# Kernel optimization log

Hardware: AMD Instinct MI355X
Metric: run time of the kernel (lower is better)

Reference implementation:

```python
import jax, jax.numpy as jnp
import numpy as np

HIDDEN = 1024
NUM_HEADS = 16
HEAD_DIM = HIDDEN // NUM_HEADS
ROPE_THETA = 10000.0


def rope_tables(seq_len, head_dim, theta):
    inv_freq = 1.0 / theta ** (jnp.arange(0, head_dim, 2, dtype=jnp.float32) / head_dim)
    pos = jnp.arange(seq_len, dtype=jnp.float32)
    freqs = jnp.outer(pos, inv_freq)  # [S, hd/2]
    return jnp.cos(freqs), jnp.sin(freqs)


def apply_rope(x, cos, sin):
    # x: [B, nh, S, hd]; cos/sin: [S, hd/2]
    x1, x2 = jnp.split(x, 2, axis=-1)
    return jnp.concatenate([x1 * cos - x2 * sin, x2 * cos + x1 * sin], axis=-1)


def setup_inputs() -> dict:
    key = jax.random.key(0)
    k1, k2, k3 = jax.random.split(key, 3)
    B, S = 2, 2048
    hidden_states = jax.random.normal(k1, (B, S, HIDDEN), dtype=jnp.float32)
    # nn.Linear stores weight as [out, in]; y = x @ W.T
    Wqkv = jax.random.normal(k2, (3 * HIDDEN, HIDDEN), dtype=jnp.float32) * (HIDDEN ** -0.5)
    Wo = jax.random.normal(k3, (HIDDEN, HIDDEN), dtype=jnp.float32) * (HIDDEN ** -0.5)
    return {"hidden_states": hidden_states, "Wqkv": Wqkv, "Wo": Wo}


def reference(hidden_states, Wqkv, Wo):
    B, S, H = hidden_states.shape
    qkv = hidden_states @ Wqkv.T  # [B, S, 3H]
    qkv = qkv.reshape(B, S, 3, NUM_HEADS, HEAD_DIM)
    q, k, v = jnp.moveaxis(qkv, 2, 0)  # each [B, S, nh, hd]
    q = jnp.transpose(q, (0, 2, 1, 3))  # [B, nh, S, hd]
    k = jnp.transpose(k, (0, 2, 1, 3))
    v = jnp.transpose(v, (0, 2, 1, 3))
    cos, sin = rope_tables(S, HEAD_DIM, ROPE_THETA)
    q = apply_rope(q, cos, sin)
    k = apply_rope(k, cos, sin)
    scale = 1.0 / jnp.sqrt(jnp.asarray(HEAD_DIM, dtype=q.dtype))
    scores = jnp.einsum("bhqd,bhkd->bhqk", q, k) * scale
    causal = jnp.tril(jnp.ones((S, S), dtype=bool))
    scores = jnp.where(causal, scores, jnp.finfo(scores.dtype).min)
    attn = jax.nn.softmax(scores, axis=-1)
    out = jnp.einsum("bhqk,bhkd->bhqd", attn, v)  # [B, nh, S, hd]
    out = jnp.transpose(out, (0, 2, 1, 3)).reshape(B, S, H)
    return out @ Wo.T
```

## Files before the change

### kernel.cpp

```cpp
#include <hip/hip_runtime.h>
#include <hip/hip_bf16.h>
#include <math.h>

typedef __bf16 bf16_t;
typedef __attribute__((ext_vector_type(8))) __bf16 bf16x8;
typedef __attribute__((ext_vector_type(4))) float f32x4;
typedef __attribute__((ext_vector_type(16))) float f32x16;
typedef __attribute__((ext_vector_type(4))) unsigned u32x4;

#define AS1(p) ((__attribute__((address_space(1))) void*)(p))
#define AS3(p) ((__attribute__((address_space(3))) void*)(p))

__global__ void cvt_f32_bf16(const float* __restrict__ in, bf16_t* __restrict__ out, int n8) {
  int i = blockIdx.x * blockDim.x + threadIdx.x;
  if (i >= n8) return;
  const float4* p = (const float4*)in;
  float4 a = p[2 * i], b = p[2 * i + 1];
  bf16x8 o;
  o[0] = (bf16_t)a.x; o[1] = (bf16_t)a.y; o[2] = (bf16_t)a.z; o[3] = (bf16_t)a.w;
  o[4] = (bf16_t)b.x; o[5] = (bf16_t)b.y; o[6] = (bf16_t)b.z; o[7] = (bf16_t)b.w;
  ((bf16x8*)out)[i] = o;
}

__global__ void rope_tables_k(float* __restrict__ cosb, float* __restrict__ sinb) {
  int t = blockIdx.x * 256 + threadIdx.x;
  int s = t >> 5, i = t & 31;
  float inv = powf(10000.0f, -(float)i / 32.0f);
  float ang = (float)s * inv;
  float sv, cv;
  sincosf(ang, &sv, &cv);
  cosb[t] = cv;
  sinb[t] = sv;
}

__global__ __launch_bounds__(256)
void pack_rope(bf16_t* __restrict__ qkv, const float* __restrict__ cosb,
               const float* __restrict__ sinb, bf16_t* __restrict__ Kp) {
  __shared__ bf16_t vl[64][72];
  const int t = blockIdx.x, bh = blockIdx.y, b = bh >> 4, h = bh & 15;
  const int tid = threadIdx.x;
  const int r = tid >> 2, j = tid & 3;
  const int s = t * 64 + r;
  bf16_t* base = qkv + ((size_t)(b * 2048 + s)) * 3072 + h * 64;
  const float* cb = cosb + s * 32 + j * 8;
  const float* sb = sinb + s * 32 + j * 8;
  bf16x8 q1 = *(const bf16x8*)(base + j * 8);
  bf16x8 q2 = *(const bf16x8*)(base + j * 8 + 32);
  bf16x8 k1 = *(const bf16x8*)(base + 1024 + j * 8);
  bf16x8 k2 = *(const bf16x8*)(base + 1024 + j * 8 + 32);
  bf16x8 v1 = *(const bf16x8*)(base + 2048 + j * 8);
  bf16x8 v2 = *(const bf16x8*)(base + 2048 + j * 8 + 32);
  const float QS = 0.125f * 1.4426950408889634f;
  bf16x8 qo1, qo2, ko1, ko2;
#pragma unroll
  for (int i = 0; i < 8; ++i) {
    float c = cb[i], sn = sb[i];
    float a1 = (float)q1[i], a2 = (float)q2[i];
    qo1[i] = (bf16_t)((a1 * c - a2 * sn) * QS);
    qo2[i] = (bf16_t)((a2 * c + a1 * sn) * QS);
    float b1 = (float)k1[i], b2 = (float)k2[i];
    ko1[i] = (bf16_t)(b1 * c - b2 * sn);
    ko2[i] = (bf16_t)(b2 * c + b1 * sn);
  }
  *(bf16x8*)(base + j * 8) = qo1;
  *(bf16x8*)(base + j * 8 + 32) = qo2;
  bf16_t* kd = Kp + ((size_t)(bh * 32 + t)) * 4096 + r * 64;
  *(bf16x8*)(kd + ((j ^ (r & 7)) * 8)) = ko1;
  *(bf16x8*)(kd + (((j + 4) ^ (r & 7)) * 8)) = ko2;
#pragma unroll
  for (int i = 0; i < 8; ++i) { vl[r][j * 8 + i] = v1[i]; vl[r][j * 8 + 32 + i] = v2[i]; }
  __syncthreads();
  const int d = r;
  bf16x8 o1, o2;
#pragma unroll
  for (int i = 0; i < 8; ++i) { o1[i] = vl[j * 16 + i][d]; o2[i] = vl[j * 16 + 8 + i][d]; }
  bf16_t* vd = base + 2048;
  *(bf16x8*)(vd + (((2 * j) ^ (d & 7)) * 8)) = o1;
  *(bf16x8*)(vd + (((2 * j + 1) ^ (d & 7)) * 8)) = o2;
}

template <typename OutT>
__global__ __launch_bounds__(256, 2)
void gemm_nt(const bf16_t* __restrict__ A, const bf16_t* __restrict__ B,
             OutT* __restrict__ C, int M, int N, int K) {
  __shared__ __align__(16) bf16_t lA[128 * 64];
  __shared__ __align__(16) bf16_t lB[128 * 64];
  const int tid = threadIdx.x;
  const int wid = tid >> 6, lane = tid & 63;
  const int lr = lane & 15, lg = lane >> 4;
  const int nwg = gridDim.x * gridDim.y;
  int lin = blockIdx.y * gridDim.x + blockIdx.x;
  lin = (lin & 7) * (nwg >> 3) + (lin >> 3);
  const int m0 = (lin / gridDim.x) * 128, n0 = (lin % gridDim.x) * 128;
  const int wm = (wid >> 1) * 64, wn = (wid & 1) * 64;
  const int srow = lane >> 3;
  const int scol = (lane & 7) * 8;
  f32x4 acc[4][4];
#pragma unroll
  for (int i = 0; i < 4; ++i)
#pragma unroll
    for (int j = 0; j < 4; ++j) acc[i][j] = f32x4{0.f, 0.f, 0.f, 0.f};

  const int nk = K >> 6;
  for (int kt = 0; kt < nk; ++kt) {
    const int k0 = kt << 6;
    __syncthreads();
#pragma unroll
    for (int i = 0; i < 4; ++i) {
      int c = (wid << 2) + i;
      int r = (c << 3) + srow;
      __builtin_amdgcn_global_load_lds(AS1(A + (size_t)(m0 + r) * K + k0 + scol),
                                       AS3(&lA[c * 512]), 16, 0, 0);
      __builtin_amdgcn_global_load_lds(AS1(B + (size_t)(n0 + r) * K + k0 + scol),
                                       AS3(&lB[c * 512]), 16, 0, 0);
    }
    __syncthreads();
#pragma unroll
    for (int ks = 0; ks < 2; ++ks) {
      bf16x8 af[4], bfr[4];
#pragma unroll
      for (int i = 0; i < 4; ++i) {
        af[i]  = *(const bf16x8*)&lA[(wm + i * 16 + lr) * 64 + ks * 32 + lg * 8];
        bfr[i] = *(const bf16x8*)&lB[(wn + i * 16 + lr) * 64 + ks * 32 + lg * 8];
      }
#pragma unroll
      for (int i = 0; i < 4; ++i)
#pragma unroll
        for (int j = 0; j < 4; ++j)
          acc[i][j] = __builtin_amdgcn_mfma_f32_16x16x32_bf16(af[i], bfr[j], acc[i][j], 0, 0, 0);
    }
  }
#pragma unroll
  for (int i = 0; i < 4; ++i)
#pragma unroll
    for (int j = 0; j < 4; ++j)
#pragma unroll
      for (int r = 0; r < 4; ++r) {
        int row = m0 + wm + i * 16 + lg * 4 + r;
        int col = n0 + wn + j * 16 + lr;
        C[(size_t)row * N + col] = (OutT)acc[i][j][r];
      }
}

__device__ inline unsigned pkbf(float a, float b) {
  bf16_t x = (bf16_t)a, y = (bf16_t)b;
  return (unsigned)__builtin_bit_cast(unsigned short, x) |
         ((unsigned)__builtin_bit_cast(unsigned short, y) << 16);
}
__device__ inline f32x16 zero16() {
  f32x16 z;
#pragma unroll
  for (int r = 0; r < 16; ++r) z[r] = 0.f;
  return z;
}

__global__ __launch_bounds__(128, 1)
void attn_fwd(const bf16_t* __restrict__ qkv, const bf16_t* __restrict__ Kp,
              bf16_t* __restrict__ O) {
  __shared__ __align__(16) bf16_t Ksh[2][4096];
  __shared__ __align__(16) bf16_t Vsh[2][4096];
  const int tid = threadIdx.x, wid = tid >> 6, lane = tid & 63;
  const int ln = lane & 31, h = lane >> 5;
  const int lin = blockIdx.y * 16 + blockIdx.x;
  const int c = (lin >> 3) & 15;
  const int bh = (lin & 7) | ((lin >> 7) << 3);
  const int b = bh >> 4, hd = bh & 15;
  const int cA = c, cB = 31 - c;
  const int NI = 33;

  const bf16_t* QArow = qkv + ((size_t)(b * 2048 + cA * 64 + wid * 32 + ln)) * 3072 + hd * 64;
  const bf16_t* QBrow = qkv + ((size_t)(b * 2048 + cB * 64 + wid * 32 + ln)) * 3072 + hd * 64;
  bf16x8 qA[4], qB[4], qc[4];
#pragma unroll
  for (int t = 0; t < 4; ++t) {
    qA[t] = *(const bf16x8*)(QArow + t * 16 + h * 8);
    qB[t] = *(const bf16x8*)(QBrow + t * 16 + h * 8);
    qc[t] = qA[t];
  }
  int qwc = cA * 64 + wid * 32;

  f32x16 o0 = zero16(), o1 = zero16();
  float lp = 0.f;

  const bf16_t* Kbase = Kp + ((size_t)bh * 32) * 4096 + tid * 8;
  const bf16_t* Vbase = qkv + ((size_t)(b * 2048 + (tid >> 3))) * 3072 + 2048 + hd * 64 + (tid & 7) * 8;

#define TILE_OF(IT) ((IT) <= c ? (IT) : (IT) - (c + 1))
#define STAGE(IT, BUF)                                                                    \
  do {                                                                                    \
    int _t = TILE_OF(IT);                                                                 \
    const bf16_t* ks = Kbase + (size_t)_t * 4096;                                         \
    __builtin_amdgcn_global_load_lds(AS1(ks),        AS3(&Ksh[BUF][tid * 8]), 16, 0, 0);  \
    __builtin_amdgcn_global_load_lds(AS1(ks + 1024), AS3(&Ksh[BUF][1024 + tid * 8]), 16, 0, 0); \
    __builtin_amdgcn_global_load_lds(AS1(ks + 2048), AS3(&Ksh[BUF][2048 + tid * 8]), 16, 0, 0); \
    __builtin_amdgcn_global_load_lds(AS1(ks + 3072), AS3(&Ksh[BUF][3072 + tid * 8]), 16, 0, 0); \
    const bf16_t* vs = Vbase + (size_t)_t * 64 * 3072;                                    \
    __builtin_amdgcn_global_load_lds(AS1(vs),             AS3(&Vsh[BUF][tid * 8]), 16, 0, 0);        \
    __builtin_amdgcn_global_load_lds(AS1(vs + 16 * 3072), AS3(&Vsh[BUF][1024 + tid * 8]), 16, 0, 0); \
    __builtin_amdgcn_global_load_lds(AS1(vs + 32 * 3072), AS3(&Vsh[BUF][2048 + tid * 8]), 16, 0, 0); \
    __builtin_amdgcn_global_load_lds(AS1(vs + 48 * 3072), AS3(&Vsh[BUF][3072 + tid * 8]), 16, 0, 0); \
  } while (0)

  STAGE(0, 0);
  for (int i = 0; i < NI; ++i) {
    asm volatile("s_waitcnt vmcnt(0)" ::: "memory");
    __builtin_amdgcn_s_barrier();
    if (i + 1 < NI) STAGE(i + 1, (i + 1) & 1);
    const bf16_t* K = &Ksh[i & 1][0];
    const bf16_t* V = &Vsh[i & 1][0];
    f32x16 s0 = zero16(), s1 = zero16();
    __builtin_amdgcn_s_setprio(1);
#pragma unroll
    for (int t = 0; t < 4; ++t) {
      const int ch = 2 * t + h;
      bf16x8 k0 = *(const bf16x8*)&K[ln * 64 + ((ch ^ (ln & 7)) * 8)];
      bf16x8 k1 = *(const bf16x8*)&K[(32 + ln) * 64 + ((ch ^ (ln & 7)) * 8)];
      s0 = __builtin_amdgcn_mfma_f32_32x32x16_bf16(k0, qc[t], s0, 0, 0, 0);
      s1 = __builtin_amdgcn_mfma_f32_32x32x16_bf16(k1, qc[t], s1, 0, 0, 0);
    }
    __builtin_amdgcn_s_setprio(0);
    if (i == c || i == NI - 1) {
      int qg = qwc + ln;
      int k0g = TILE_OF(i) * 64;
#pragma unroll
      for (int r = 0; r < 16; ++r) {
        int kv = k0g + (r & 3) + 8 * (r >> 2) + 4 * h;
        if (kv > qg) s0[r] = -3e38f;
        if (kv + 32 > qg) s1[r] = -3e38f;
      }
    }
#pragma unroll
    for (int r = 0; r < 16; ++r) {
      float p0 = __builtin_amdgcn_exp2f(s0[r]); lp += p0; s0[r] = p0;
      float p1 = __builtin_amdgcn_exp2f(s1[r]); lp += p1; s1[r] = p1;
    }
    __builtin_amdgcn_s_setprio(1);
#pragma unroll
    for (int t = 0; t < 4; ++t) {
      const int u = t & 1;
      f32x16 sv = (t >> 1) ? s1 : s0;
      unsigned x  = pkbf(sv[8 * u + 0], sv[8 * u + 1]);
      unsigned x2 = pkbf(sv[8 * u + 2], sv[8 * u + 3]);
      unsigned y  = pkbf(sv[8 * u + 4], sv[8 * u + 5]);
      unsigned y2 = pkbf(sv[8 * u + 6], sv[8 * u + 7]);
      asm volatile("v_permlane32_swap_b32 %0, %1" : "+v"(x), "+v"(y));
      asm volatile("v_permlane32_swap_b32 %0, %1" : "+v"(x2), "+v"(y2));
      u32x4 pw; pw[0] = x; pw[1] = x2; pw[2] = y; pw[3] = y2;
      bf16x8 pf = __builtin_bit_cast(bf16x8, pw);
      const int ch = 2 * t + h;
      bf16x8 v0 = *(const bf16x8*)&V[ln * 64 + ((ch ^ (ln & 7)) * 8)];
      bf16x8 v1 = *(const bf16x8*)&V[(32 + ln) * 64 + ((ch ^ (ln & 7)) * 8)];
      o0 = __builtin_amdgcn_mfma_f32_32x32x16_bf16(v0, pf, o0, 0, 0, 0);
      o1 = __builtin_amdgcn_mfma_f32_32x32x16_bf16(v1, pf, o1, 0, 0, 0);
    }
    __builtin_amdgcn_s_setprio(0);
    if (i == c) {
      float lpf = lp + __shfl_xor(lp, 32, 64);
      float inv = 1.0f / lpf;
      bf16_t* Oaddr = O + ((size_t)(b * 2048 + qwc + ln)) * 1024 + hd * 64;
#pragma unroll
      for (int D = 0; D < 2; ++D) {
        f32x16 ov = D ? o1 : o0;
#pragma unroll
        for (int Q = 0; Q < 4; ++Q) {
          uint2 w;
          w.x = pkbf(ov[4 * Q + 0] * inv, ov[4 * Q + 1] * inv);
          w.y = pkbf(ov[4 * Q + 2] * inv, ov[4 * Q + 3] * inv);
          *(uint2*)(Oaddr + D * 32 + Q * 8 + 4 * h) = w;
        }
      }
      o0 = zero16(); o1 = zero16(); lp = 0.f;
#pragma unroll
      for (int t = 0; t < 4; ++t) qc[t] = qB[t];
      qwc = cB * 64 + wid * 32;
    }
  }
#undef STAGE
#undef TILE_OF
  {
    float lpf = lp + __shfl_xor(lp, 32, 64);
    float inv = 1.0f / lpf;
    bf16_t* Oaddr = O + ((size_t)(b * 2048 + qwc + ln)) * 1024 + hd * 64;
#pragma unroll
    for (int D = 0; D < 2; ++D) {
      f32x16 ov = D ? o1 : o0;
#pragma unroll
      for (int Q = 0; Q < 4; ++Q) {
        uint2 w;
        w.x = pkbf(ov[4 * Q + 0] * inv, ov[4 * Q + 1] * inv);
        w.y = pkbf(ov[4 * Q + 2] * inv, ov[4 * Q + 3] * inv);
        *(uint2*)(Oaddr + D * 32 + Q * 8 + 4 * h) = w;
      }
    }
  }
}

extern "C" void kernel_launch(void* const* d_in, const int* in_sizes, int n_in,
                              void* d_out, int out_size, void* d_ws, size_t ws_size,
                              hipStream_t stream) {
  const float* hid  = (const float*)d_in[0];
  const float* wqkv = (const float*)d_in[1];
  const float* wo   = (const float*)d_in[2];
  float* out = (float*)d_out;
  char* ws = (char*)d_ws;
  bf16_t* hidb  = (bf16_t*)(ws);
  bf16_t* wqkvb = (bf16_t*)(ws + 8388608);
  bf16_t* wob   = (bf16_t*)(ws + 14680064);
  bf16_t* qkvb  = (bf16_t*)(ws + 16777216);
  float*  cosb  = (float*)(ws + 41943040);
  float*  sinb  = (float*)(ws + 42205184);
  bf16_t* Ob    = (bf16_t*)(ws + 42467328);
  bf16_t* Kp    = (bf16_t*)(ws);

  cvt_f32_bf16<<<2048, 256, 0, stream>>>(hid, hidb, 524288);
  cvt_f32_bf16<<<1536, 256, 0, stream>>>(wqkv, wqkvb, 393216);
  cvt_f32_bf16<<<512, 256, 0, stream>>>(wo, wob, 131072);
  rope_tables_k<<<256, 256, 0, stream>>>(cosb, sinb);
  gemm_nt<bf16_t><<<dim3(24, 32), 256, 0, stream>>>(hidb, wqkvb, qkvb, 4096, 3072, 1024);
  pack_rope<<<dim3(32, 32), 256, 0, stream>>>(qkvb, cosb, sinb, Kp);
  attn_fwd<<<dim3(16, 32), 128, 0, stream>>>(qkvb, Kp, Ob);
  gemm_nt<float><<<dim3(8, 32), 256, 0, stream>>>(Ob, wob, out, 4096, 1024, 1024);
}
```

Before: 140.2 us.

## Fuse prep kernels and split paired causal attention blocks into longest-first tiles

Merges the three f32-to-bf16 conversions and the RoPE table kernel into one launch to cut launch overhead. Replaces the paired query-tile scheme (each block handling tiles c and 31-c, 33 iterations) with one query tile per block, 1024 blocks in a heavy-first interleaved order. Also allows two blocks per CU through launch bounds. The intent is better load balance and occupancy from finer-grained work, at the cost of reloading each Q tile once per block and giving up the fixed-length pairing.

New measurement: 122.0 us. 1.15x faster.

```diff
diff --git a/kernel.cpp b/kernel.cpp
--- a/kernel.cpp
+++ b/kernel.cpp
@@ -11,9 +11,7 @@
 #define AS1(p) ((__attribute__((address_space(1))) void*)(p))
 #define AS3(p) ((__attribute__((address_space(3))) void*)(p))
 
-__global__ void cvt_f32_bf16(const float* __restrict__ in, bf16_t* __restrict__ out, int n8) {
-  int i = blockIdx.x * blockDim.x + threadIdx.x;
-  if (i >= n8) return;
+__device__ inline void cvt8(const float* __restrict__ in, bf16_t* __restrict__ out, int i) {
   const float4* p = (const float4*)in;
   float4 a = p[2 * i], b = p[2 * i + 1];
   bf16x8 o;
@@ -22,15 +20,27 @@
   ((bf16x8*)out)[i] = o;
 }
 
-__global__ void rope_tables_k(float* __restrict__ cosb, float* __restrict__ sinb) {
-  int t = blockIdx.x * 256 + threadIdx.x;
-  int s = t >> 5, i = t & 31;
-  float inv = powf(10000.0f, -(float)i / 32.0f);
-  float ang = (float)s * inv;
-  float sv, cv;
-  sincosf(ang, &sv, &cv);
-  cosb[t] = cv;
-  sinb[t] = sv;
+__global__ __launch_bounds__(256)
+void prep_all(const float* __restrict__ hid, const float* __restrict__ wqkv,
+              const float* __restrict__ wo, bf16_t* __restrict__ hidb,
+              bf16_t* __restrict__ wqkvb, bf16_t* __restrict__ wob,
+              float* __restrict__ cosb, float* __restrict__ sinb) {
+  const int bid = blockIdx.x, tid = threadIdx.x;
+  if (bid < 2048) {
+    cvt8(hid, hidb, bid * 256 + tid);
+  } else if (bid < 3584) {
+    cvt8(wqkv, wqkvb, (bid - 2048) * 256 + tid);
+  } else if (bid < 4096) {
+    cvt8(wo, wob, (bid - 3584) * 256 + tid);
+  } else {
+    int t = (bid - 4096) * 256 + tid;
+    int s = t >> 5, i = t & 31;
+    float inv = powf(10000.0f, -(float)i / 32.0f);
+    float sv, cv;
+    sincosf((float)s * inv, &sv, &cv);
+    cosb[t] = cv;
+    sinb[t] = sv;
+  }
 }
 
 __global__ __launch_bounds__(256)
@@ -154,30 +164,25 @@
   return z;
 }
 
-__global__ __launch_bounds__(128, 1)
+__global__ __launch_bounds__(128, 2)
 void attn_fwd(const bf16_t* __restrict__ qkv, const bf16_t* __restrict__ Kp,
               bf16_t* __restrict__ O) {
   __shared__ __align__(16) bf16_t Ksh[2][4096];
   __shared__ __align__(16) bf16_t Vsh[2][4096];
   const int tid = threadIdx.x, wid = tid >> 6, lane = tid & 63;
   const int ln = lane & 31, h = lane >> 5;
-  const int lin = blockIdx.y * 16 + blockIdx.x;
-  const int c = (lin >> 3) & 15;
-  const int bh = (lin & 7) | ((lin >> 7) << 3);
+  const int lin = blockIdx.x;
+  const int g = lin >> 8, j = lin & 255;
+  const int bh = j & 31, cc = j >> 5;
+  const int c = (g == 0) ? 31 - cc : (g == 1) ? 16 + cc : (g == 2) ? 15 - cc : cc;
   const int b = bh >> 4, hd = bh & 15;
-  const int cA = c, cB = 31 - c;
-  const int NI = 33;
-
-  const bf16_t* QArow = qkv + ((size_t)(b * 2048 + cA * 64 + wid * 32 + ln)) * 3072 + hd * 64;
-  const bf16_t* QBrow = qkv + ((size_t)(b * 2048 + cB * 64 + wid * 32 + ln)) * 3072 + hd * 64;
-  bf16x8 qA[4], qB[4], qc[4];
-#pragma unroll
-  for (int t = 0; t < 4; ++t) {
-    qA[t] = *(const bf16x8*)(QArow + t * 16 + h * 8);
-    qB[t] = *(const bf16x8*)(QBrow + t * 16 + h * 8);
-    qc[t] = qA[t];
-  }
-  int qwc = cA * 64 + wid * 32;
+  const int NI = c + 1;
+  const int qw = c * 64 + wid * 32;
+
+  const bf16_t* Qrow = qkv + ((size_t)(b * 2048 + qw + ln)) * 3072 + hd * 64;
+  bf16x8 qf[4];
+#pragma unroll
+  for (int t = 0; t < 4; ++t) qf[t] = *(const bf16x8*)(Qrow + t * 16 + h * 8);
 
   f32x16 o0 = zero16(), o1 = zero16();
   float lp = 0.f;
@@ -185,16 +190,14 @@
   const bf16_t* Kbase = Kp + ((size_t)bh * 32) * 4096 + tid * 8;
   const bf16_t* Vbase = qkv + ((size_t)(b * 2048 + (tid >> 3))) * 3072 + 2048 + hd * 64 + (tid & 7) * 8;
 
-#define TILE_OF(IT) ((IT) <= c ? (IT) : (IT) - (c + 1))
-#define STAGE(IT, BUF)                                                                    \
+#define STAGE(T, BUF)                                                                     \
   do {                                                                                    \
-    int _t = TILE_OF(IT);                                                                 \
-    const bf16_t* ks = Kbase + (size_t)_t * 4096;                                         \
+    const bf16_t* ks = Kbase + (size_t)(T) * 4096;                                        \
     __builtin_amdgcn_global_load_lds(AS1(ks),        AS3(&Ksh[BUF][tid * 8]), 16, 0, 0);  \
     __builtin_amdgcn_global_load_lds(AS1(ks + 1024), AS3(&Ksh[BUF][1024 + tid * 8]), 16, 0, 0); \
     __builtin_amdgcn_global_load_lds(AS1(ks + 2048), AS3(&Ksh[BUF][2048 + tid * 8]), 16, 0, 0); \
     __builtin_amdgcn_global_load_lds(AS1(ks + 3072), AS3(&Ksh[BUF][3072 + tid * 8]), 16, 0, 0); \
-    const bf16_t* vs = Vbase + (size_t)_t * 64 * 3072;                                    \
+    const bf16_t* vs = Vbase + (size_t)(T) * 64 * 3072;                                   \
     __builtin_amdgcn_global_load_lds(AS1(vs),             AS3(&Vsh[BUF][tid * 8]), 16, 0, 0);        \
     __builtin_amdgcn_global_load_lds(AS1(vs + 16 * 3072), AS3(&Vsh[BUF][1024 + tid * 8]), 16, 0, 0); \
     __builtin_amdgcn_global_load_lds(AS1(vs + 32 * 3072), AS3(&Vsh[BUF][2048 + tid * 8]), 16, 0, 0); \
@@ -215,13 +218,12 @@
       const int ch = 2 * t + h;
       bf16x8 k0 = *(const bf16x8*)&K[ln * 64 + ((ch ^ (ln & 7)) * 8)];
       bf16x8 k1 = *(const bf16x8*)&K[(32 + ln) * 64 + ((ch ^ (ln & 7)) * 8)];
-      s0 = __builtin_amdgcn_mfma_f32_32x32x16_bf16(k0, qc[t], s0, 0, 0, 0);
-      s1 = __builtin_amdgcn_mfma_f32_32x32x16_bf16(k1, qc[t], s1, 0, 0, 0);
+      s0 = __builtin_amdgcn_mfma_f32_32x32x16_bf16(k0, qf[t], s0, 0, 0, 0);
+      s1 = __builtin_amdgcn_mfma_f32_32x32x16_bf16(k1, qf[t], s1, 0, 0, 0);
     }
     __builtin_amdgcn_s_setprio(0);
-    if (i == c || i == NI - 1) {
-      int qg = qwc + ln;
-      int k0g = TILE_OF(i) * 64;
+    if (i == NI - 1) {
+      const int qg = qw + ln, k0g = i * 64;
 #pragma unroll
       for (int r = 0; r < 16; ++r) {
         int kv = k0g + (r & 3) + 8 * (r >> 2) + 4 * h;
@@ -254,33 +256,12 @@
       o1 = __builtin_amdgcn_mfma_f32_32x32x16_bf16(v1, pf, o1, 0, 0, 0);
     }
     __builtin_amdgcn_s_setprio(0);
-    if (i == c) {
-      float lpf = lp + __shfl_xor(lp, 32, 64);
-      float inv = 1.0f / lpf;
-      bf16_t* Oaddr = O + ((size_t)(b * 2048 + qwc + ln)) * 1024 + hd * 64;
-#pragma unroll
-      for (int D = 0; D < 2; ++D) {
-        f32x16 ov = D ? o1 : o0;
-#pragma unroll
-        for (int Q = 0; Q < 4; ++Q) {
-          uint2 w;
-          w.x = pkbf(ov[4 * Q + 0] * inv, ov[4 * Q + 1] * inv);
-          w.y = pkbf(ov[4 * Q + 2] * inv, ov[4 * Q + 3] * inv);
-          *(uint2*)(Oaddr + D * 32 + Q * 8 + 4 * h) = w;
-        }
-      }
-      o0 = zero16(); o1 = zero16(); lp = 0.f;
-#pragma unroll
-      for (int t = 0; t < 4; ++t) qc[t] = qB[t];
-      qwc = cB * 64 + wid * 32;
-    }
   }
 #undef STAGE
-#undef TILE_OF
   {
     float lpf = lp + __shfl_xor(lp, 32, 64);
     float inv = 1.0f / lpf;
-    bf16_t* Oaddr = O + ((size_t)(b * 2048 + qwc + ln)) * 1024 + hd * 64;
+    bf16_t* Oaddr = O + ((size_t)(b * 2048 + qw + ln)) * 1024 + hd * 64;
 #pragma unroll
     for (int D = 0; D < 2; ++D) {
       f32x16 ov = D ? o1 : o0;
@@ -312,12 +293,9 @@
   bf16_t* Ob    = (bf16_t*)(ws + 42467328);
   bf16_t* Kp    = (bf16_t*)(ws);
 
-  cvt_f32_bf16<<<2048, 256, 0, stream>>>(hid, hidb, 524288);
-  cvt_f32_bf16<<<1536, 256, 0, stream>>>(wqkv, wqkvb, 393216);
-  cvt_f32_bf16<<<512, 256, 0, stream>>>(wo, wob, 131072);
-  rope_tables_k<<<256, 256, 0, stream>>>(cosb, sinb);
+  prep_all<<<4352, 256, 0, stream>>>(hid, wqkv, wo, hidb, wqkvb, wob, cosb, sinb);
   gemm_nt<bf16_t><<<dim3(24, 32), 256, 0, stream>>>(hidb, wqkvb, qkvb, 4096, 3072, 1024);
   pack_rope<<<dim3(32, 32), 256, 0, stream>>>(qkvb, cosb, sinb, Kp);
-  attn_fwd<<<dim3(16, 32), 128, 0, stream>>>(qkvb, Kp, Ob);
+  attn_fwd<<<1024, 128, 0, stream>>>(qkvb, Kp, Ob);
   gemm_nt<float><<<dim3(8, 32), 256, 0, stream>>>(Ob, wob, out, 4096, 1024, 1024);
 }
```
